# Kernel tuning notes

Measured on AMD Instinct MI355X. Metric: run time of the kernel, lower is better.

Reference implementation:

```python
import jax, jax.numpy as jnp
import numpy as np

B, H, W, C = 16, 56, 56, 384
WS, SHIFT, NH = 8, 4, 12
HID = 4 * C
N = WS * WS
EPS = 1e-5


def _rel_index():
    coords = np.stack(np.meshgrid(np.arange(WS), np.arange(WS), indexing='ij')).reshape(2, -1)
    rel = coords[:, :, None] - coords[:, None, :]
    rel = rel.transpose(1, 2, 0).astype(np.int32)
    rel[..., 0] += WS - 1
    rel[..., 1] += WS - 1
    rel[..., 0] *= 2 * WS - 1
    return rel.sum(-1)  # [N, N]


def _attn_mask():
    img = np.zeros((H, W))
    bounds = [(0, H - WS), (H - WS, H - SHIFT), (H - SHIFT, H)]
    cnt = 0
    for h0, h1 in bounds:
        for w0, w1 in bounds:
            img[h0:h1, w0:w1] = cnt
            cnt += 1
    mw = img.reshape(H // WS, WS, W // WS, WS).transpose(0, 2, 1, 3).reshape(-1, N)
    am = mw[:, None, :] - mw[:, :, None]
    return np.where(am != 0, -100.0, 0.0).astype(np.float32)  # [nW, N, N]


def setup_inputs() -> dict:
    key = jax.random.key(0)
    ks = jax.random.split(key, 12)
    s = lambda k, shp, sc=0.02: (jax.random.normal(k, shp, jnp.float32) * sc)
    return {
        'x': jax.random.normal(ks[0], (B, H * W, C), jnp.float32),
        'norm1_g': jnp.ones((C,), jnp.float32),
        'norm1_b': jnp.zeros((C,), jnp.float32),
        'qkv_w': s(ks[1], (C, 3 * C)),
        'qkv_b': jnp.zeros((3 * C,), jnp.float32),
        'proj_w': s(ks[2], (C, C)),
        'proj_b': jnp.zeros((C,), jnp.float32),
        'rel_bias': s(ks[3], ((2 * WS - 1) * (2 * WS - 1), NH)),
        'norm2_g': jnp.ones((C,), jnp.float32),
        'norm2_b': jnp.zeros((C,), jnp.float32),
        'fc1_w': s(ks[4], (C, HID)),
        'fc1_b': jnp.zeros((HID,), jnp.float32),
        'fc2_w': s(ks[5], (HID, C)),
        'fc2_b': jnp.zeros((C,), jnp.float32),
        'rel_index': jnp.asarray(_rel_index()),
        'attn_mask': jnp.asarray(_attn_mask()),
    }


def _ln(x, g, b):
    mu = x.mean(-1, keepdims=True)
    var = ((x - mu) ** 2).mean(-1, keepdims=True)
    return (x - mu) * jax.lax.rsqrt(var + EPS) * g + b


def reference(x, norm1_g, norm1_b, qkv_w, qkv_b, proj_w, proj_b, rel_bias,
              norm2_g, norm2_b, fc1_w, fc1_b, fc2_w, fc2_b, rel_index, attn_mask):
    hd = C // NH
    scale = hd ** -0.5
    shortcut = x
    h = _ln(x, norm1_g, norm1_b).reshape(B, H, W, C)
    h = jnp.roll(h, (-SHIFT, -SHIFT), axis=(1, 2))
    # window partition -> [B*nW, N, C]
    xw = h.reshape(B, H // WS, WS, W // WS, WS, C).transpose(0, 1, 3, 2, 4, 5).reshape(-1, N, C)
    B_ = xw.shape[0]
    qkv = (xw @ qkv_w + qkv_b).reshape(B_, N, 3, NH, hd).transpose(2, 0, 3, 1, 4)
    q, k, v = qkv[0], qkv[1], qkv[2]  # [B_, NH, N, hd]
    attn = jnp.einsum('bhid,bhjd->bhij', q * scale, k)
    bias = rel_bias[rel_index.reshape(-1)].reshape(N, N, NH).transpose(2, 0, 1)  # [NH, N, N]
    attn = attn + bias[None]
    nW = attn_mask.shape[0]
    attn = attn.reshape(B_ // nW, nW, NH, N, N) + attn_mask[None, :, None]
    attn = attn.reshape(B_, NH, N, N)
    attn = jax.nn.softmax(attn, axis=-1)
    out = jnp.einsum('bhij,bhjd->bhid', attn, v).transpose(0, 2, 1, 3).reshape(B_, N, C)
    out = out @ proj_w + proj_b
    # window reverse
    out = out.reshape(B, H // WS, W // WS, WS, WS, C).transpose(0, 1, 3, 2, 4, 5).reshape(B, H, W, C)
    out = jnp.roll(out, (SHIFT, SHIFT), axis=(1, 2)).reshape(B, H * W, C)
    y = shortcut + out
    h2 = _ln(y, norm2_g, norm2_b)
    mlp = jax.nn.gelu(h2 @ fc1_w + fc1_b, approximate=False) @ fc2_w + fc2_b
    y = y + mlp
    return (y, attn)
```

## Files before the change

### kernel.cpp

```cpp
#include <hip/hip_runtime.h>
#include <hip/hip_bf16.h>
#include <math.h>

#define ROWS 50176

typedef short s16;
typedef unsigned int u32;
typedef __attribute__((ext_vector_type(4))) float f32x4;
typedef __attribute__((ext_vector_type(8))) short s16x8;
typedef __attribute__((ext_vector_type(8))) __bf16 bf16x8;

typedef __attribute__((address_space(1))) const u32 gu32;
typedef __attribute__((address_space(3))) u32 lu32;

__device__ __forceinline__ void gload16(const void* g, void* l) {
  __builtin_amdgcn_global_load_lds((gu32*)g, (lu32*)l, 16, 0, 0);
}

__device__ __forceinline__ s16 f2bf(float f) {
  unsigned u = __float_as_uint(f);
  u = (u + 0x7fffu + ((u >> 16) & 1u)) >> 16;
  return (s16)u;
}

__global__ void convT(const float* __restrict__ src, s16* __restrict__ dst, int K, int N) {
  int i = blockIdx.x * 256 + threadIdx.x;
  if (i >= K * N) return;
  int n = i / K, k = i - n * K;
  dst[i] = f2bf(src[(size_t)k * N + n]);
}

__global__ __launch_bounds__(256) void ln_k(const float* __restrict__ x,
    const float* __restrict__ g, const float* __restrict__ b,
    s16* __restrict__ out, int window_map) {
  int r = blockIdx.x * 4 + (threadIdx.x >> 6);
  int lane = threadIdx.x & 63;
  size_t src;
  if (window_map) {
    int w = r >> 6, t = r & 63;
    int bb = w / 49, wi = w - bb * 49;
    int wh = wi / 7, ww = wi - wh * 7;
    int i = (wh * 8 + (t >> 3) + 4) % 56;
    int j = (ww * 8 + (t & 7) + 4) % 56;
    src = (size_t)bb * 3136 + i * 56 + j;
  } else {
    src = (size_t)r;
  }
  const float* xr = x + src * 384;
  float v[6];
  float s = 0.f;
#pragma unroll
  for (int e = 0; e < 6; ++e) { v[e] = xr[lane + e * 64]; s += v[e]; }
#pragma unroll
  for (int o = 1; o < 64; o <<= 1) s += __shfl_xor(s, o, 64);
  float mu = s * (1.f / 384.f);
  float q = 0.f;
#pragma unroll
  for (int e = 0; e < 6; ++e) { float d = v[e] - mu; q += d * d; }
#pragma unroll
  for (int o = 1; o < 64; o <<= 1) q += __shfl_xor(q, o, 64);
  float rs = rsqrtf(q * (1.f / 384.f) + 1e-5f);
  s16* orow = out + (size_t)r * 384;
#pragma unroll
  for (int e = 0; e < 6; ++e) {
    int c = lane + e * 64;
    orow[c] = f2bf((v[e] - mu) * rs * g[c] + b[c]);
  }
}

template<int EPI>
__global__ __launch_bounds__(512, 2) void gemm_bt(const s16* __restrict__ A,
    const s16* __restrict__ BT, const float* __restrict__ bias, int K, int N,
    s16* __restrict__ obf, float* of, const float* res) {
  __shared__ s16 smem[2][(256 + 192) * 64];
  const int t = threadIdx.x;
  const int nbx = N / 192;
  const int nwg = gridDim.x;
  int id = blockIdx.x;
  const int q8 = nwg >> 3, r8 = nwg & 7;
  const int xcd = id & 7, loc = id >> 3;
  const int swz = (xcd < r8 ? xcd * (q8 + 1) : r8 * (q8 + 1) + (xcd - r8) * q8) + loc;
  const int by = swz / nbx, bx = swz - by * nbx;
  const int m0 = by * 256, n0 = bx * 192;

  const int wv = t >> 6, lane = t & 63;
  const int wr = wv >> 1, wc = wv & 1;
  const int lr = lane & 15, lg = lane >> 4;

  const s16* asrc[4]; const s16* bsrc[3];
  int aofs[4], bofs[3];
#pragma unroll
  for (int i = 0; i < 4; ++i) {
    int o = (i * 512 + t) * 16;
    int row = o >> 7, pc = (o >> 4) & 7, lc = pc ^ (row & 7);
    aofs[i] = o;
    asrc[i] = A + (size_t)(m0 + row) * K + lc * 8;
  }
#pragma unroll
  for (int i = 0; i < 3; ++i) {
    int o = (i * 512 + t) * 16;
    int row = o >> 7, pc = (o >> 4) & 7, lc = pc ^ (row & 7);
    bofs[i] = o + 256 * 128;
    bsrc[i] = BT + (size_t)(n0 + row) * K + lc * 8;
  }

  f32x4 acc[4][6] = {};

#pragma unroll
  for (int i = 0; i < 4; ++i) gload16(asrc[i], (char*)&smem[0][0] + aofs[i]);
#pragma unroll
  for (int i = 0; i < 3; ++i) gload16(bsrc[i], (char*)&smem[0][0] + bofs[i]);

  int cur = 0;
  for (int k0 = 0; k0 < K; k0 += 64) {
    if (k0 + 64 < K) {
#pragma unroll
      for (int i = 0; i < 4; ++i) gload16(asrc[i] + k0 + 64, (char*)&smem[cur ^ 1][0] + aofs[i]);
#pragma unroll
      for (int i = 0; i < 3; ++i) gload16(bsrc[i] + k0 + 64, (char*)&smem[cur ^ 1][0] + bofs[i]);
      __builtin_amdgcn_sched_barrier(0);
      asm volatile("s_waitcnt vmcnt(7)" ::: "memory");
    } else {
      __builtin_amdgcn_sched_barrier(0);
      asm volatile("s_waitcnt vmcnt(0)" ::: "memory");
    }
    __builtin_amdgcn_s_barrier();
    __builtin_amdgcn_sched_barrier(0);

    const char* Ab = (const char*)&smem[cur][0];
    const char* Bb = Ab + 256 * 128;
    bf16x8 af[2][4], bv[2][6];
#pragma unroll
    for (int kk = 0; kk < 2; ++kk) {
      const int cbase = kk * 4 + lg;
#pragma unroll
      for (int m = 0; m < 4; ++m) {
        int ar = wr * 64 + m * 16 + lr;
        af[kk][m] = *reinterpret_cast<const bf16x8*>(Ab + ar * 128 + (cbase ^ (ar & 7)) * 16);
      }
#pragma unroll
      for (int n = 0; n < 6; ++n) {
        int br = wc * 96 + n * 16 + lr;
        bv[kk][n] = *reinterpret_cast<const bf16x8*>(Bb + br * 128 + (cbase ^ (br & 7)) * 16);
      }
    }
#pragma unroll
    for (int kk = 0; kk < 2; ++kk)
#pragma unroll
      for (int m = 0; m < 4; ++m)
#pragma unroll
        for (int n = 0; n < 6; ++n)
          acc[m][n] = __builtin_amdgcn_mfma_f32_16x16x32_bf16(af[kk][m], bv[kk][n], acc[m][n], 0, 0, 0);
    __builtin_amdgcn_sched_barrier(0);
    __builtin_amdgcn_s_barrier();
    __builtin_amdgcn_sched_barrier(0);
    cur ^= 1;
  }

#pragma unroll
  for (int m = 0; m < 4; ++m) {
#pragma unroll
    for (int r = 0; r < 4; ++r) {
      const int row = m0 + wr * 64 + m * 16 + lg * 4 + r;
      size_t drow = (size_t)row;
      if (EPI == 1) {
        int w = row >> 6, tt = row & 63;
        int bb = w / 49, wi = w - bb * 49;
        int wh = wi / 7, ww = wi - wh * 7;
        int fi = (wh * 8 + (tt >> 3) + 4) % 56;
        int fj = (ww * 8 + (tt & 7) + 4) % 56;
        drow = (size_t)bb * 3136 + fi * 56 + fj;
      }
#pragma unroll
      for (int n = 0; n < 6; ++n) {
        const int col = n0 + wc * 96 + n * 16 + lr;
        float v = acc[m][n][r] + bias[col];
        if (EPI == 0) {
          obf[(size_t)row * N + col] = f2bf(v);
        } else if (EPI == 1) {
          size_t o = drow * 384 + col;
          of[o] = res[o] + v;
        } else if (EPI == 2) {
          v = 0.5f * v * (1.f + erff(v * 0.70710678118f));
          obf[(size_t)row * N + col] = f2bf(v);
        } else {
          size_t o = (size_t)row * 384 + col;
          of[o] = res[o] + v;
        }
      }
    }
  }
}

__global__ __launch_bounds__(64) void attn_k(const s16* __restrict__ qkv,
    const float* __restrict__ rel_bias, const int* __restrict__ rel_index,
    const float* __restrict__ mask, float* __restrict__ probs, s16* __restrict__ aout) {
  __shared__ s16 VT[32][72];
  __shared__ s16 P[64][72];
  const int blk = blockIdx.x;
  const int w = blk / 12, nh = blk - w * 12;
  const int lane = threadIdx.x;
  const int lr = lane & 15, lg = lane >> 4;
  const s16* base = qkv + (size_t)w * 64 * 1152;

  {
    const s16* vrow = base + (size_t)lane * 1152 + 768 + nh * 32;
    s16x8 v0 = *reinterpret_cast<const s16x8*>(vrow);
    s16x8 v1 = *reinterpret_cast<const s16x8*>(vrow + 8);
    s16x8 v2 = *reinterpret_cast<const s16x8*>(vrow + 16);
    s16x8 v3 = *reinterpret_cast<const s16x8*>(vrow + 24);
#pragma unroll
    for (int d = 0; d < 8; ++d) {
      VT[d][lane] = v0[d];
      VT[8 + d][lane] = v1[d];
      VT[16 + d][lane] = v2[d];
      VT[24 + d][lane] = v3[d];
    }
  }

  bf16x8 qf[4], kf[4];
#pragma unroll
  for (int m = 0; m < 4; ++m)
    qf[m] = *reinterpret_cast<const bf16x8*>(base + (size_t)(m * 16 + lr) * 1152 + nh * 32 + lg * 8);
#pragma unroll
  for (int n = 0; n < 4; ++n)
    kf[n] = *reinterpret_cast<const bf16x8*>(base + (size_t)(n * 16 + lr) * 1152 + 384 + nh * 32 + lg * 8);

  f32x4 s[4][4] = {};
#pragma unroll
  for (int m = 0; m < 4; ++m)
#pragma unroll
    for (int n = 0; n < 4; ++n)
      s[m][n] = __builtin_amdgcn_mfma_f32_16x16x32_bf16(qf[m], kf[n], s[m][n], 0, 0, 0);

  const float scale = 0.1767766952966369f;
  const float* mrow = mask + (size_t)(w % 49) * 4096;
#pragma unroll
  for (int m = 0; m < 4; ++m)
#pragma unroll
    for (int n = 0; n < 4; ++n)
#pragma unroll
      for (int r = 0; r < 4; ++r) {
        int i = m * 16 + lg * 4 + r, j = n * 16 + lr;
        s[m][n][r] = s[m][n][r] * scale
                   + rel_bias[(size_t)rel_index[i * 64 + j] * 12 + nh]
                   + mrow[i * 64 + j];
      }
#pragma unroll
  for (int m = 0; m < 4; ++m)
#pragma unroll
    for (int r = 0; r < 4; ++r) {
      float mx = fmaxf(fmaxf(s[m][0][r], s[m][1][r]), fmaxf(s[m][2][r], s[m][3][r]));
#pragma unroll
      for (int o = 1; o < 16; o <<= 1) mx = fmaxf(mx, __shfl_xor(mx, o, 64));
      float sum = 0.f;
#pragma unroll
      for (int n = 0; n < 4; ++n) {
        float e = __expf(s[m][n][r] - mx);
        s[m][n][r] = e;
        sum += e;
      }
#pragma unroll
      for (int o = 1; o < 16; o <<= 1) sum += __shfl_xor(sum, o, 64);
      float inv = 1.f / sum;
#pragma unroll
      for (int n = 0; n < 4; ++n) s[m][n][r] *= inv;
    }
  float* prow = probs + (size_t)(w * 12 + nh) * 4096;
#pragma unroll
  for (int m = 0; m < 4; ++m)
#pragma unroll
    for (int n = 0; n < 4; ++n)
#pragma unroll
      for (int r = 0; r < 4; ++r) {
        int i = m * 16 + lg * 4 + r, j = n * 16 + lr;
        float pv = s[m][n][r];
        prow[i * 64 + j] = pv;
        P[i][j] = f2bf(pv);
      }
  __syncthreads();
  f32x4 o2[4][2] = {};
#pragma unroll
  for (int m = 0; m < 4; ++m)
#pragma unroll
    for (int kk = 0; kk < 2; ++kk) {
      bf16x8 pa = *reinterpret_cast<const bf16x8*>(&P[m * 16 + lr][kk * 32 + lg * 8]);
#pragma unroll
      for (int n = 0; n < 2; ++n) {
        bf16x8 vb = *reinterpret_cast<const bf16x8*>(&VT[n * 16 + lr][kk * 32 + lg * 8]);
        o2[m][n] = __builtin_amdgcn_mfma_f32_16x16x32_bf16(pa, vb, o2[m][n], 0, 0, 0);
      }
    }
#pragma unroll
  for (int m = 0; m < 4; ++m)
#pragma unroll
    for (int n = 0; n < 2; ++n)
#pragma unroll
      for (int r = 0; r < 4; ++r) {
        int i = m * 16 + lg * 4 + r, d = n * 16 + lr;
        aout[((size_t)w * 64 + i) * 384 + nh * 32 + d] = f2bf(o2[m][n][r]);
      }
}

extern "C" void kernel_launch(void* const* d_in, const int* in_sizes, int n_in,
                              void* d_out, int out_size, void* d_ws, size_t ws_size,
                              hipStream_t stream) {
  const float* x        = (const float*)d_in[0];
  const float* n1g      = (const float*)d_in[1];
  const float* n1b      = (const float*)d_in[2];
  const float* qkv_w    = (const float*)d_in[3];
  const float* qkv_b    = (const float*)d_in[4];
  const float* proj_w   = (const float*)d_in[5];
  const float* proj_b   = (const float*)d_in[6];
  const float* rel_bias = (const float*)d_in[7];
  const float* n2g      = (const float*)d_in[8];
  const float* n2b      = (const float*)d_in[9];
  const float* fc1_w    = (const float*)d_in[10];
  const float* fc1_b    = (const float*)d_in[11];
  const float* fc2_w    = (const float*)d_in[12];
  const float* fc2_b    = (const float*)d_in[13];
  const int*   rel_idx  = (const int*)d_in[14];
  const float* amask    = (const float*)d_in[15];

  float* out   = (float*)d_out;
  float* probs = out + (size_t)ROWS * 384;

  s16* wqkvT = (s16*)d_ws;
  s16* wprojT = wqkvT + 1152 * 384;
  s16* wfc1T = wprojT + 384 * 384;
  s16* wfc2T = wfc1T + 1536 * 384;
  s16* bufA = wfc2T + 384 * 1536;
  s16* bufB = bufA + (size_t)ROWS * 384;
  s16* bufC = bufB + (size_t)ROWS * 1152;

  convT<<<(1152 * 384) / 256, 256, 0, stream>>>(qkv_w, wqkvT, 384, 1152);
  convT<<<(384 * 384) / 256, 256, 0, stream>>>(proj_w, wprojT, 384, 384);
  convT<<<(1536 * 384) / 256, 256, 0, stream>>>(fc1_w, wfc1T, 384, 1536);
  convT<<<(384 * 1536) / 256, 256, 0, stream>>>(fc2_w, wfc2T, 1536, 384);

  ln_k<<<ROWS / 4, 256, 0, stream>>>(x, n1g, n1b, bufA, 1);
  gemm_bt<0><<<(1152 / 192) * (ROWS / 256), 512, 0, stream>>>(bufA, wqkvT, qkv_b, 384, 1152, bufB, nullptr, nullptr);
  attn_k<<<784 * 12, 64, 0, stream>>>(bufB, rel_bias, rel_idx, amask, probs, bufC);
  gemm_bt<1><<<(384 / 192) * (ROWS / 256), 512, 0, stream>>>(bufC, wprojT, proj_b, 384, 384, nullptr, out, x);
  ln_k<<<ROWS / 4, 256, 0, stream>>>(out, n2g, n2b, bufA, 0);
  gemm_bt<2><<<(1536 / 192) * (ROWS / 256), 512, 0, stream>>>(bufA, wfc1T, fc1_b, 384, 1536, bufB, nullptr, nullptr);
  gemm_bt<3><<<(384 / 192) * (ROWS / 256), 512, 0, stream>>>(bufB, wfc2T, fc2_b, 1536, 384, nullptr, out, out);
}
```

Before: 610.5 us.

## Restructure GEMM main loop into phased LDS reads with 2-ahead prefetch

Changes the wave tiling from a 4x2 grid of 64x96 tiles to a 2x4 grid of 128x48 tiles. The K-tile loop is split into four phases, each loading a subset of A/B fragments from LDS and issuing 12 MFMAs under raised wave priority (s_setprio) with barriers between phases. The global-to-LDS prefetch now runs two tiles ahead, issued after compute into the buffer just consumed. The goal is to overlap LDS reads and global loads with MFMA work and cut fragment register pressure, at the cost of more barriers per K step.

```diff
diff --git a/kernel.cpp b/kernel.cpp
--- a/kernel.cpp
+++ b/kernel.cpp
@@ -84,7 +84,7 @@
   const int m0 = by * 256, n0 = bx * 192;
 
   const int wv = t >> 6, lane = t & 63;
-  const int wr = wv >> 1, wc = wv & 1;
+  const int wr = wv & 1, wc = wv >> 1;
   const int lr = lane & 15, lg = lane >> 4;
 
   const s16* asrc[4]; const s16* bsrc[3];
@@ -104,24 +104,25 @@
     bsrc[i] = BT + (size_t)(n0 + row) * K + lc * 8;
   }
 
-  f32x4 acc[4][6] = {};
+  f32x4 acc[8][3] = {};
+
+  const int nt = K >> 6;
 
 #pragma unroll
   for (int i = 0; i < 4; ++i) gload16(asrc[i], (char*)&smem[0][0] + aofs[i]);
 #pragma unroll
   for (int i = 0; i < 3; ++i) gload16(bsrc[i], (char*)&smem[0][0] + bofs[i]);
+#pragma unroll
+  for (int i = 0; i < 4; ++i) gload16(asrc[i] + 64, (char*)&smem[1][0] + aofs[i]);
+#pragma unroll
+  for (int i = 0; i < 3; ++i) gload16(bsrc[i] + 64, (char*)&smem[1][0] + bofs[i]);
 
   int cur = 0;
-  for (int k0 = 0; k0 < K; k0 += 64) {
-    if (k0 + 64 < K) {
-#pragma unroll
-      for (int i = 0; i < 4; ++i) gload16(asrc[i] + k0 + 64, (char*)&smem[cur ^ 1][0] + aofs[i]);
-#pragma unroll
-      for (int i = 0; i < 3; ++i) gload16(bsrc[i] + k0 + 64, (char*)&smem[cur ^ 1][0] + bofs[i]);
-      __builtin_amdgcn_sched_barrier(0);
+  for (int tI = 0; tI < nt; ++tI) {
+    __builtin_amdgcn_sched_barrier(0);
+    if (tI + 1 < nt) {
       asm volatile("s_waitcnt vmcnt(7)" ::: "memory");
     } else {
-      __builtin_amdgcn_sched_barrier(0);
       asm volatile("s_waitcnt vmcnt(0)" ::: "memory");
     }
     __builtin_amdgcn_s_barrier();
@@ -129,39 +130,57 @@
 
     const char* Ab = (const char*)&smem[cur][0];
     const char* Bb = Ab + 256 * 128;
-    bf16x8 af[2][4], bv[2][6];
-#pragma unroll
-    for (int kk = 0; kk < 2; ++kk) {
-      const int cbase = kk * 4 + lg;
+
+    bf16x8 bfr[3], afr[4];
+#pragma unroll
+    for (int ph = 0; ph < 4; ++ph) {
+      const int ks = ph >> 1, mh = ph & 1;
+      if (mh == 0) {
+#pragma unroll
+        for (int n = 0; n < 3; ++n) {
+          int br = wc * 48 + n * 16 + lr;
+          bfr[n] = *reinterpret_cast<const bf16x8*>(
+              Bb + br * 128 + (((ks << 2) | lg) ^ (br & 7)) * 16);
+        }
+      }
 #pragma unroll
       for (int m = 0; m < 4; ++m) {
-        int ar = wr * 64 + m * 16 + lr;
-        af[kk][m] = *reinterpret_cast<const bf16x8*>(Ab + ar * 128 + (cbase ^ (ar & 7)) * 16);
-      }
-#pragma unroll
-      for (int n = 0; n < 6; ++n) {
-        int br = wc * 96 + n * 16 + lr;
-        bv[kk][n] = *reinterpret_cast<const bf16x8*>(Bb + br * 128 + (cbase ^ (br & 7)) * 16);
-      }
-    }
-#pragma unroll
-    for (int kk = 0; kk < 2; ++kk)
+        int ar = wr * 128 + (mh * 4 + m) * 16 + lr;
+        afr[m] = *reinterpret_cast<const bf16x8*>(
+            Ab + ar * 128 + (((ks << 2) | lg) ^ (ar & 7)) * 16);
+      }
+      __builtin_amdgcn_sched_barrier(0);
+      __builtin_amdgcn_s_barrier();
+      asm volatile("s_waitcnt lgkmcnt(0)" ::: "memory");
+      __builtin_amdgcn_sched_barrier(0);
+      __builtin_amdgcn_s_setprio(1);
 #pragma unroll
       for (int m = 0; m < 4; ++m)
 #pragma unroll
-        for (int n = 0; n < 6; ++n)
-          acc[m][n] = __builtin_amdgcn_mfma_f32_16x16x32_bf16(af[kk][m], bv[kk][n], acc[m][n], 0, 0, 0);
-    __builtin_amdgcn_sched_barrier(0);
-    __builtin_amdgcn_s_barrier();
-    __builtin_amdgcn_sched_barrier(0);
+        for (int n = 0; n < 3; ++n)
+          acc[mh * 4 + m][n] = __builtin_amdgcn_mfma_f32_16x16x32_bf16(
+              afr[m], bfr[n], acc[mh * 4 + m][n], 0, 0, 0);
+      __builtin_amdgcn_s_setprio(0);
+      __builtin_amdgcn_sched_barrier(0);
+      __builtin_amdgcn_s_barrier();
+      __builtin_amdgcn_sched_barrier(0);
+    }
+
+    if (tI + 2 < nt) {
+      const int k0 = (tI + 2) << 6;
+#pragma unroll
+      for (int i = 0; i < 4; ++i) gload16(asrc[i] + k0, (char*)&smem[cur][0] + aofs[i]);
+#pragma unroll
+      for (int i = 0; i < 3; ++i) gload16(bsrc[i] + k0, (char*)&smem[cur][0] + bofs[i]);
+    }
     cur ^= 1;
   }
 
 #pragma unroll
-  for (int m = 0; m < 4; ++m) {
+  for (int mf = 0; mf < 8; ++mf) {
 #pragma unroll
     for (int r = 0; r < 4; ++r) {
-      const int row = m0 + wr * 64 + m * 16 + lg * 4 + r;
+      const int row = m0 + wr * 128 + mf * 16 + lg * 4 + r;
       size_t drow = (size_t)row;
       if (EPI == 1) {
         int w = row >> 6, tt = row & 63;
@@ -172,9 +191,9 @@
         drow = (size_t)bb * 3136 + fi * 56 + fj;
       }
 #pragma unroll
-      for (int n = 0; n < 6; ++n) {
-        const int col = n0 + wc * 96 + n * 16 + lr;
-        float v = acc[m][n][r] + bias[col];
+      for (int n = 0; n < 3; ++n) {
+        const int col = n0 + wc * 48 + n * 16 + lr;
+        float v = acc[mf][n][r] + bias[col];
         if (EPI == 0) {
           obf[(size_t)row * N + col] = f2bf(v);
         } else if (EPI == 1) {
```

Measured after the change: 624.8 us. +2.4%, slower.
